# Optimization experiments

Hardware: AMD Instinct MI355X
Metric: run time of the kernel (lower is better)

## Reference

```python
import jax, jax.numpy as jnp
import numpy as np

B, N, C = 256, 128, 607

def setup_inputs() -> dict:
    key = jax.random.key(0)
    k1, k2 = jax.random.split(key)
    obj_sem_cls_pred = jax.random.normal(k1, (B, N, C), dtype=jnp.float32)
    # labels in [-1, C): negative entries mean 'ignore' (stay all-zero)
    obj_labels = jax.random.randint(k2, (B, N), -1, C, dtype=jnp.int64)
    return {
        "obj_sem_cls_pred": obj_sem_cls_pred,
        "obj_labels": obj_labels,
        "cur_step": 1000,
        "total_steps": 10000,
    }

def reference(obj_sem_cls_pred, obj_labels, cur_step, total_steps):
    # Fused masked one-hot: replaces the B*N Python-loop scatter.
    # Rows with obj_labels < 0 remain all zeros.
    valid = (obj_labels >= 0)[..., None]  # [B, N, 1]
    onehot = jax.nn.one_hot(jnp.maximum(obj_labels, 0),
                            obj_sem_cls_pred.shape[-1],
                            dtype=obj_sem_cls_pred.dtype)  # [B, N, C]
    return jnp.where(valid, onehot, jnp.zeros_like(onehot))
```

## Files before the change

### kernel.cpp

```cpp
#include <hip/hip_runtime.h>
#include <hip/hip_bf16.h>


#define BB 256
#define NN 128
#define CC 607
#define TOTAL (BB * NN * CC)
#define NV4   (TOTAL / 4)

__global__ __launch_bounds__(256) void fill_zero_kernel(float4* __restrict__ out) {
    const float4 z = make_float4(0.f, 0.f, 0.f, 0.f);
    int base = blockIdx.x * 1024 + threadIdx.x;
    out[base]       = z;
    out[base + 256] = z;
    out[base + 512] = z;
    out[base + 768] = z;
}

__global__ __launch_bounds__(256) void scatter_ones_kernel(const int* __restrict__ labels,
                                                           float* __restrict__ out) {
    int t = blockIdx.x * 256 + threadIdx.x;
    int lab = labels[t];
    if (lab >= 0)
        out[t * CC + lab] = 1.0f;
}

extern "C" void kernel_launch(void* const* d_in, const int* in_sizes, int n_in,
                              void* d_out, int out_size, void* d_ws, size_t ws_size,
                              hipStream_t stream) {
    const int* labels = (const int*)d_in[1];
    float* out = (float*)d_out;

    fill_zero_kernel<<<NV4 / 1024, 256, 0, stream>>>((float4*)out);
    scatter_ones_kernel<<<(BB * NN) / 256, 256, 0, stream>>>(labels, out);
}
```

Before: 18.62 us.

## Fuse zero-fill and one-hot scatter into a single kernel

Merges the zero-fill and scatter kernels into one launch. Each block zeroes its own 4096-float chunk, synchronizes, and then up to 8 threads write the 1.0 for any rows whose label position falls inside that chunk. This removes the second kernel launch and the dependency between the two kernels. In exchange every block pays a barrier and a small serialized tail of label reads.

```diff
diff --git a/kernel.cpp b/kernel.cpp
--- a/kernel.cpp
+++ b/kernel.cpp
@@ -5,24 +5,39 @@
 #define BB 256
 #define NN 128
 #define CC 607
-#define TOTAL (BB * NN * CC)
+#define NROWS (BB * NN)
+#define TOTAL (NROWS * CC)
 #define NV4   (TOTAL / 4)
+#define NBLOCKS (NV4 / 1024)
 
-__global__ __launch_bounds__(256) void fill_zero_kernel(float4* __restrict__ out) {
+__global__ __launch_bounds__(256) void onehot_fused_kernel(const int* __restrict__ labels,
+                                                           float* __restrict__ out) {
+    const int b = blockIdx.x;
+    const int tid = threadIdx.x;
+
+    float4* o4 = reinterpret_cast<float4*>(out) + b * 1024 + tid;
     const float4 z = make_float4(0.f, 0.f, 0.f, 0.f);
-    int base = blockIdx.x * 1024 + threadIdx.x;
-    out[base]       = z;
-    out[base + 256] = z;
-    out[base + 512] = z;
-    out[base + 768] = z;
-}
+    o4[0]   = z;
+    o4[256] = z;
+    o4[512] = z;
+    o4[768] = z;
 
-__global__ __launch_bounds__(256) void scatter_ones_kernel(const int* __restrict__ labels,
-                                                           float* __restrict__ out) {
-    int t = blockIdx.x * 256 + threadIdx.x;
-    int lab = labels[t];
-    if (lab >= 0)
-        out[t * CC + lab] = 1.0f;
+    __syncthreads();
+
+    if (tid < 8) {
+        const int lo = b * 4096;
+        const int hi = lo + 4096;
+        unsigned rlo = (unsigned)lo / (unsigned)CC;
+        unsigned r = rlo + tid;
+        if (r < NROWS && (int)(r * CC) < hi) {
+            int lab = labels[r];
+            if (lab >= 0) {
+                int flat = (int)(r * CC) + lab;
+                if (flat >= lo && flat < hi)
+                    out[flat] = 1.0f;
+            }
+        }
+    }
 }
 
 extern "C" void kernel_launch(void* const* d_in, const int* in_sizes, int n_in,
@@ -31,6 +46,5 @@
     const int* labels = (const int*)d_in[1];
     float* out = (float*)d_out;
 
-    fill_zero_kernel<<<NV4 / 1024, 256, 0, stream>>>((float4*)out);
-    scatter_ones_kernel<<<(BB * NN) / 256, 256, 0, stream>>>(labels, out);
+    onehot_fused_kernel<<<NBLOCKS, 256, 0, stream>>>(labels, out);
 }
```

After: 16.94 us, median of 2. -9.0%, faster.
